# Optimization experiments

Hardware: AMD Instinct MI355X
Metric: run time of the kernel (lower is better)

Reference implementation:

```python
import jax, jax.numpy as jnp
import numpy as np

NUM_HEADS = 16
DIM = 1024


def setup_inputs() -> dict:
    key = jax.random.key(0)
    kx, kw, kb = jax.random.split(key, 3)
    x = jax.random.normal(kx, (4, 2048, DIM), dtype=jnp.float32)
    # torch Linear(dim, 3*dim): weight [3d, d], bias [3d]; store as [d, 3d] for x @ W
    W_qkv = jax.random.normal(kw, (DIM, 3 * DIM), dtype=jnp.float32) * (1.0 / np.sqrt(DIM))
    b_qkv = jax.random.normal(kb, (3 * DIM,), dtype=jnp.float32) * 0.01
    return {"x": x, "W_qkv": W_qkv, "b_qkv": b_qkv}


def reference(x, W_qkv, b_qkv):
    b, t, d = x.shape
    h = NUM_HEADS
    hd = d // h
    qkv = x @ W_qkv + b_qkv  # [b, t, 3d]
    q, k, v = jnp.split(qkv, 3, axis=-1)
    # [b, t, h, hd] -> [b, h, t, hd]
    q = q.reshape(b, t, h, hd).transpose(0, 2, 1, 3)
    k = k.reshape(b, t, h, hd).transpose(0, 2, 1, 3)
    v = v.reshape(b, t, h, hd).transpose(0, 2, 1, 3)
    # NOTE: original scales by sqrt(full dim d), not head_dim
    logits = jnp.einsum("bhqc,bhkc->bhqk", q, k) / jnp.sqrt(jnp.float32(d))
    causal = jnp.tril(jnp.ones((t, t), dtype=bool))  # [t, t]
    logits = jnp.where(causal, logits, -jnp.inf)
    attn = jax.nn.softmax(logits, axis=-1)
    out = jnp.einsum("bhqk,bhkc->bhqc", attn, v)  # [b, h, t, hd]
    return out.transpose(0, 2, 1, 3).reshape(b, t, d)
```

## Files before the change

kernel.cpp:

```cpp
#include <hip/hip_runtime.h>
#include <hip/hip_bf16.h>

#define D_MODEL 1024
#define N3      3072
#define TSEQ    2048
#define M_TOT   8192

typedef __bf16 bf16_8 __attribute__((ext_vector_type(8)));
typedef float  f32x4  __attribute__((ext_vector_type(4)));
typedef short  s16x4  __attribute__((ext_vector_type(4)));

static __device__ __forceinline__ unsigned short f2bf(float f) {
  __hip_bfloat16 h = __float2bfloat16(f);
  unsigned short u;
  __builtin_memcpy(&u, &h, 2);
  return u;
}
static __device__ __forceinline__ unsigned pack2(float lo, float hi) {
  return (unsigned)f2bf(lo) | ((unsigned)f2bf(hi) << 16);
}
static __device__ __forceinline__ void gload16(const void* g, void* l) {
  __builtin_amdgcn_global_load_lds((const __attribute__((address_space(1))) void*)g,
                                   (__attribute__((address_space(3))) void*)l, 16, 0, 0);
}

__global__ void cvt_x_kernel(const float* __restrict__ x, __bf16* __restrict__ xb) {
  size_t i = (size_t)blockIdx.x * 256 + threadIdx.x;
  float4 v = *(const float4*)(x + i * 4);
  ushort4 o;
  o.x = f2bf(v.x); o.y = f2bf(v.y); o.z = f2bf(v.z); o.w = f2bf(v.w);
  *(ushort4*)((unsigned short*)xb + i * 4) = o;
}

__global__ void cvt_w_kernel(const float* __restrict__ W, __bf16* __restrict__ WT) {
  __shared__ unsigned short tl[64][68];
  int t = threadIdx.x;
  int n0 = blockIdx.x * 64, k0 = blockIdx.y * 64;
  int rr = t >> 4, cc = (t & 15) * 4;
#pragma unroll
  for (int i = 0; i < 4; ++i) {
    int r = rr + i * 16;
    float4 v = *(const float4*)(W + (size_t)(k0 + r) * N3 + n0 + cc);
    tl[r][cc] = f2bf(v.x); tl[r][cc + 1] = f2bf(v.y);
    tl[r][cc + 2] = f2bf(v.z); tl[r][cc + 3] = f2bf(v.w);
  }
  __syncthreads();
#pragma unroll
  for (int i = 0; i < 4; ++i) {
    int rc = rr + i * 16;
    ushort4 o;
    o.x = tl[cc + 0][rc]; o.y = tl[cc + 1][rc];
    o.z = tl[cc + 2][rc]; o.w = tl[cc + 3][rc];
    *(ushort4*)((unsigned short*)WT + (size_t)(n0 + rc) * D_MODEL + k0 + cc) = o;
  }
}

__global__ void vtrans_kernel(const __bf16* __restrict__ qkv, __bf16* __restrict__ VT) {
  __shared__ unsigned short tl[64][68];
  int t = threadIdx.x;
  int t0 = blockIdx.x * 64;
  int bh = blockIdx.y;
  int b = bh >> 4, h = bh & 15;
  int rr = t >> 4, cc = (t & 15) * 4;
  const unsigned short* q16 = (const unsigned short*)qkv;
#pragma unroll
  for (int i = 0; i < 4; ++i) {
    int r = rr + i * 16;
    ushort4 v = *(const ushort4*)(q16 + (size_t)(b * TSEQ + t0 + r) * N3 + 2048 + h * 64 + cc);
    tl[r][cc] = v.x; tl[r][cc + 1] = v.y; tl[r][cc + 2] = v.z; tl[r][cc + 3] = v.w;
  }
  __syncthreads();
#pragma unroll
  for (int i = 0; i < 4; ++i) {
    int rc = rr + i * 16;
    ushort4 o;
    o.x = tl[cc + 0][rc]; o.y = tl[cc + 1][rc];
    o.z = tl[cc + 2][rc]; o.w = tl[cc + 3][rc];
    *(ushort4*)((unsigned short*)VT + (size_t)(bh * 64 + rc) * TSEQ + t0 + cc) = o;
  }
}

__global__ __launch_bounds__(256, 2) void gemm_qkv_kernel(
    const __bf16* __restrict__ A, const __bf16* __restrict__ Bt,
    const float* __restrict__ bias, __bf16* __restrict__ C) {
  __shared__ __align__(16) __bf16 Al[4][4096];
  __shared__ __align__(16) __bf16 Bl[4][4096];
  int tid = threadIdx.x;
  int wave = tid >> 6, lane = tid & 63;
  int lr = lane & 15, lg = lane >> 4;
  int m0 = blockIdx.x * 128, n0 = blockIdx.y * 128;
  int wm = (wave >> 1) * 64, wn = (wave & 1) * 64;

  const f32x4 fz = {0.f, 0.f, 0.f, 0.f};
  f32x4 acc[4][4];
#pragma unroll
  for (int i = 0; i < 4; ++i)
#pragma unroll
    for (int j = 0; j < 4; ++j) acc[i][j] = fz;

  auto stage = [&](int buf, int kt) {
#pragma unroll
    for (int call = 0; call < 2; ++call) {
      int cb = call * 256 + wave * 64;
      int c = cb + lane;
      int row = c >> 2;
      int cir = (c & 3) ^ ((row >> 1) & 3);
      gload16(A + (size_t)(m0 + row) * D_MODEL + kt * 32 + cir * 8, &Al[buf][cb * 8]);
      gload16(Bt + (size_t)(n0 + row) * D_MODEL + kt * 32 + cir * 8, &Bl[buf][cb * 8]);
    }
  };

  stage(0, 0); stage(1, 1);
  asm volatile("s_waitcnt vmcnt(4)" ::: "memory");
  __builtin_amdgcn_sched_barrier(0);
  __builtin_amdgcn_s_barrier();

  for (int kt = 0; kt < 32; ++kt) {
    if (kt + 2 < 32) {
      stage((kt + 2) & 3, kt + 2);
      asm volatile("s_waitcnt vmcnt(8)" ::: "memory");
    } else if (kt + 1 < 32) {
      asm volatile("s_waitcnt vmcnt(4)" ::: "memory");
    } else {
      asm volatile("s_waitcnt vmcnt(0)" ::: "memory");
    }
    __builtin_amdgcn_sched_barrier(0);
    __builtin_amdgcn_s_barrier();

    int buf = kt & 3;
    bf16_8 af[4], bv[4];
#pragma unroll
    for (int mb = 0; mb < 4; ++mb) {
      int row = wm + mb * 16 + lr;
      int cir = lg ^ ((row >> 1) & 3);
      af[mb] = *(const bf16_8*)&Al[buf][row * 32 + cir * 8];
    }
#pragma unroll
    for (int nb = 0; nb < 4; ++nb) {
      int row = wn + nb * 16 + lr;
      int cir = lg ^ ((row >> 1) & 3);
      bv[nb] = *(const bf16_8*)&Bl[buf][row * 32 + cir * 8];
    }
    __builtin_amdgcn_s_setprio(1);
#pragma unroll
    for (int mb = 0; mb < 4; ++mb)
#pragma unroll
      for (int nb = 0; nb < 4; ++nb)
        acc[mb][nb] = __builtin_amdgcn_mfma_f32_16x16x32_bf16(af[mb], bv[nb], acc[mb][nb], 0, 0, 0);
    __builtin_amdgcn_s_setprio(0);
  }

  const float SC = 0.04508422f;
  float oscale = (n0 < 1024) ? SC : 1.0f;
  float bvs[4];
#pragma unroll
  for (int nb = 0; nb < 4; ++nb) bvs[nb] = bias[n0 + wn + nb * 16 + lr];
  unsigned short* C16 = (unsigned short*)C;
#pragma unroll
  for (int mb = 0; mb < 4; ++mb)
#pragma unroll
    for (int nb = 0; nb < 4; ++nb)
#pragma unroll
      for (int r = 0; r < 4; ++r) {
        int row = m0 + wm + mb * 16 + lg * 4 + r;
        int col = n0 + wn + nb * 16 + lr;
        C16[(size_t)row * N3 + col] = f2bf((acc[mb][nb][r] + bvs[nb]) * oscale);
      }
}

__global__ __launch_bounds__(256, 4) void attn_kernel(
    const __bf16* __restrict__ qkv, const __bf16* __restrict__ VT,
    float* __restrict__ out) {
  __shared__ __align__(16) char smem[32768];

  int lin = blockIdx.x;
  int y = lin & 63;
  int qt = 31 - (lin >> 6);
  int bh = (y & 7) * 8 + (y >> 3);
  int b = bh >> 4, h = bh & 15;
  int tid = threadIdx.x, wave = tid >> 6, lane = tid & 63;
  int lr = lane & 15, lg = lane >> 4;
  int q0 = qt * 64 + wave * 16;

  const __bf16* Kg = qkv + (size_t)b * TSEQ * N3 + 1024 + h * 64;
  const __bf16* Vg = VT + (size_t)bh * 64 * TSEQ;

  auto stage = [&](int buf, int kv0) {
    __bf16* Kl = (__bf16*)(smem + buf * 16384);
    __bf16* Vl = (__bf16*)(smem + buf * 16384 + 8192);
#pragma unroll
    for (int call = 0; call < 2; ++call) {
      int cb = call * 256 + wave * 64;
      int c = cb + lane;
      int row = c >> 3;
      int cir = (c & 7) ^ (row & 7);
      gload16(Kg + (size_t)(kv0 + row) * N3 + cir * 8, Kl + cb * 8);
      gload16(Vg + (size_t)row * TSEQ + kv0 + cir * 8, Vl + cb * 8);
    }
  };

  bf16_8 qf[2];
#pragma unroll
  for (int kk = 0; kk < 2; ++kk)
    qf[kk] = *(const bf16_8*)&qkv[(size_t)(b * TSEQ + q0 + lr) * N3 + h * 64 + kk * 32 + lg * 8];

  float ps_acc = 0.f;
  const f32x4 fz = {0.f, 0.f, 0.f, 0.f};
  f32x4 oacc[4];
#pragma unroll
  for (int i = 0; i < 4; ++i) oacc[i] = fz;

  int ntiles = qt + 1;
  stage(0, 0);
  asm volatile("s_waitcnt vmcnt(0)" ::: "memory");
  __builtin_amdgcn_sched_barrier(0);
  __builtin_amdgcn_s_barrier();

  for (int tt = 0; tt < ntiles; ++tt) {
    int cur = tt & 1;
    if (tt + 1 < ntiles) stage(cur ^ 1, (tt + 1) * 64);
    __builtin_amdgcn_sched_barrier(0);

    const __bf16* Kb = (const __bf16*)(smem + cur * 16384);
    const __bf16* Vb = (const __bf16*)(smem + cur * 16384 + 8192);
    int kv0 = tt * 64;
    f32x4 st[4];
#pragma unroll
    for (int i = 0; i < 4; ++i) st[i] = fz;
#pragma unroll
    for (int kk = 0; kk < 2; ++kk) {
      bf16_8 kf[4];
#pragma unroll
      for (int mb = 0; mb < 4; ++mb) {
        int row = mb * 16 + lr;
        int cir = (kk * 4 + lg) ^ (row & 7);
        kf[mb] = *(const bf16_8*)&Kb[row * 64 + cir * 8];
      }
      __builtin_amdgcn_s_setprio(1);
#pragma unroll
      for (int mb = 0; mb < 4; ++mb)
        st[mb] = __builtin_amdgcn_mfma_f32_16x16x32_bf16(kf[mb], qf[kk], st[mb], 0, 0, 0);
      __builtin_amdgcn_s_setprio(0);
    }
    unsigned pw[4][2];
    if (kv0 + 63 > q0) {
#pragma unroll
      for (int mb = 0; mb < 4; ++mb) {
        float p[4];
#pragma unroll
        for (int r = 0; r < 4; ++r) {
          int kv = kv0 + mb * 16 + lg * 4 + r;
          float s = (kv > q0 + lr) ? -1e30f : st[mb][r];
          p[r] = __builtin_amdgcn_exp2f(s);
          ps_acc += p[r];
        }
        pw[mb][0] = pack2(p[0], p[1]);
        pw[mb][1] = pack2(p[2], p[3]);
      }
    } else {
#pragma unroll
      for (int mb = 0; mb < 4; ++mb) {
        float p[4];
#pragma unroll
        for (int r = 0; r < 4; ++r) {
          p[r] = __builtin_amdgcn_exp2f(st[mb][r]);
          ps_acc += p[r];
        }
        pw[mb][0] = pack2(p[0], p[1]);
        pw[mb][1] = pack2(p[2], p[3]);
      }
    }
#pragma unroll
    for (int mb = 0; mb < 4; ++mb) {
      s16x4 vf[4];
      int chunk = mb * 2 + (lg >> 1);
#pragma unroll
      for (int mbc = 0; mbc < 4; ++mbc) {
        int row = mbc * 16 + lr;
        int cir = chunk ^ (row & 7);
        vf[mbc] = *(const s16x4*)((const char*)Vb + row * 128 + cir * 16 + (lg & 1) * 8);
      }
      union { unsigned u[2]; s16x4 v; } pf;
      pf.u[0] = pw[mb][0];
      pf.u[1] = pw[mb][1];
      __builtin_amdgcn_s_setprio(1);
#pragma unroll
      for (int mbc = 0; mbc < 4; ++mbc)
        oacc[mbc] = __builtin_amdgcn_mfma_f32_16x16x16bf16_1k(vf[mbc], pf.v, oacc[mbc], 0, 0, 0);
      __builtin_amdgcn_s_setprio(0);
    }

    if (tt + 1 < ntiles) {
      asm volatile("s_waitcnt vmcnt(0)" ::: "memory");
      __builtin_amdgcn_sched_barrier(0);
      __builtin_amdgcn_s_barrier();
    }
  }

  ps_acc += __shfl_xor(ps_acc, 16, 64);
  ps_acc += __shfl_xor(ps_acc, 32, 64);
  float invl = 1.f / ps_acc;
  float* dst = out + (size_t)(b * TSEQ + q0 + lr) * D_MODEL + h * 64 + lg * 4;
#pragma unroll
  for (int mbc = 0; mbc < 4; ++mbc) {
    float4 v;
    v.x = oacc[mbc][0] * invl; v.y = oacc[mbc][1] * invl;
    v.z = oacc[mbc][2] * invl; v.w = oacc[mbc][3] * invl;
    *(float4*)(dst + mbc * 16) = v;
  }
}

extern "C" void kernel_launch(void* const* d_in, const int* in_sizes, int n_in,
                              void* d_out, int out_size, void* d_ws, size_t ws_size,
                              hipStream_t stream) {
  const float* x = (const float*)d_in[0];
  const float* W = (const float*)d_in[1];
  const float* bias = (const float*)d_in[2];
  float* out = (float*)d_out;
  char* ws = (char*)d_ws;
  __bf16* xb  = (__bf16*)(ws);
  __bf16* WT  = (__bf16*)(ws + (size_t)16777216);
  __bf16* qkv = (__bf16*)(ws + (size_t)23068672);
  __bf16* VT  = (__bf16*)(ws + (size_t)73400320);

  hipLaunchKernelGGL(cvt_x_kernel, dim3(8192), dim3(256), 0, stream, x, xb);
  hipLaunchKernelGGL(cvt_w_kernel, dim3(48, 16), dim3(256), 0, stream, W, WT);
  hipLaunchKernelGGL(gemm_qkv_kernel, dim3(64, 24), dim3(256), 0, stream, xb, WT, bias, qkv);
  hipLaunchKernelGGL(vtrans_kernel, dim3(32, 64), dim3(256), 0, stream, qkv, VT);
  hipLaunchKernelGGL(attn_kernel, dim3(2048), dim3(256), 0, stream, qkv, VT, out);
}
```

Baseline: 148.8 us.

## Double attention query tile per block and simplify GEMM pipeline to double buffering

```diff
diff --git a/kernel.cpp b/kernel.cpp
--- a/kernel.cpp
+++ b/kernel.cpp
@@ -83,8 +83,8 @@
 __global__ __launch_bounds__(256, 2) void gemm_qkv_kernel(
     const __bf16* __restrict__ A, const __bf16* __restrict__ Bt,
     const float* __restrict__ bias, __bf16* __restrict__ C) {
-  __shared__ __align__(16) __bf16 Al[4][4096];
-  __shared__ __align__(16) __bf16 Bl[4][4096];
+  __shared__ __align__(16) __bf16 Al[2][4096];
+  __shared__ __align__(16) __bf16 Bl[2][4096];
   int tid = threadIdx.x;
   int wave = tid >> 6, lane = tid & 63;
   int lr = lane & 15, lg = lane >> 4;
@@ -110,24 +110,11 @@
     }
   };
 
-  stage(0, 0); stage(1, 1);
-  asm volatile("s_waitcnt vmcnt(4)" ::: "memory");
-  __builtin_amdgcn_sched_barrier(0);
-  __builtin_amdgcn_s_barrier();
-
+  stage(0, 0);
+  __syncthreads();
   for (int kt = 0; kt < 32; ++kt) {
-    if (kt + 2 < 32) {
-      stage((kt + 2) & 3, kt + 2);
-      asm volatile("s_waitcnt vmcnt(8)" ::: "memory");
-    } else if (kt + 1 < 32) {
-      asm volatile("s_waitcnt vmcnt(4)" ::: "memory");
-    } else {
-      asm volatile("s_waitcnt vmcnt(0)" ::: "memory");
-    }
-    __builtin_amdgcn_sched_barrier(0);
-    __builtin_amdgcn_s_barrier();
-
-    int buf = kt & 3;
+    int buf = kt & 1;
+    if (kt + 1 < 32) stage(buf ^ 1, kt + 1);
     bf16_8 af[4], bv[4];
 #pragma unroll
     for (int mb = 0; mb < 4; ++mb) {
@@ -141,13 +128,12 @@
       int cir = lg ^ ((row >> 1) & 3);
       bv[nb] = *(const bf16_8*)&Bl[buf][row * 32 + cir * 8];
     }
-    __builtin_amdgcn_s_setprio(1);
 #pragma unroll
     for (int mb = 0; mb < 4; ++mb)
 #pragma unroll
       for (int nb = 0; nb < 4; ++nb)
         acc[mb][nb] = __builtin_amdgcn_mfma_f32_16x16x32_bf16(af[mb], bv[nb], acc[mb][nb], 0, 0, 0);
-    __builtin_amdgcn_s_setprio(0);
+    __syncthreads();
   }
 
   const float SC = 0.04508422f;
@@ -175,12 +161,12 @@
 
   int lin = blockIdx.x;
   int y = lin & 63;
-  int qt = 31 - (lin >> 6);
+  int qt = 15 - (lin >> 6);
   int bh = (y & 7) * 8 + (y >> 3);
   int b = bh >> 4, h = bh & 15;
   int tid = threadIdx.x, wave = tid >> 6, lane = tid & 63;
   int lr = lane & 15, lg = lane >> 4;
-  int q0 = qt * 64 + wave * 16;
+  int q0 = qt * 128 + wave * 32;
 
   const __bf16* Kg = qkv + (size_t)b * TSEQ * N3 + 1024 + h * 64;
   const __bf16* Vg = VT + (size_t)bh * 64 * TSEQ;
@@ -199,18 +185,20 @@
     }
   };
 
-  bf16_8 qf[2];
-#pragma unroll
-  for (int kk = 0; kk < 2; ++kk)
-    qf[kk] = *(const bf16_8*)&qkv[(size_t)(b * TSEQ + q0 + lr) * N3 + h * 64 + kk * 32 + lg * 8];
-
-  float ps_acc = 0.f;
+  bf16_8 qf[2][2];
+#pragma unroll
+  for (int nb = 0; nb < 2; ++nb)
+#pragma unroll
+    for (int kk = 0; kk < 2; ++kk)
+      qf[nb][kk] = *(const bf16_8*)&qkv[(size_t)(b * TSEQ + q0 + nb * 16 + lr) * N3 + h * 64 + kk * 32 + lg * 8];
+
+  float ps[2] = {0.f, 0.f};
   const f32x4 fz = {0.f, 0.f, 0.f, 0.f};
-  f32x4 oacc[4];
-#pragma unroll
-  for (int i = 0; i < 4; ++i) oacc[i] = fz;
-
-  int ntiles = qt + 1;
+  f32x4 oacc[4][2];
+#pragma unroll
+  for (int i = 0; i < 4; ++i) { oacc[i][0] = fz; oacc[i][1] = fz; }
+
+  int ntiles = (qt + 1) * 2;
   stage(0, 0);
   asm volatile("s_waitcnt vmcnt(0)" ::: "memory");
   __builtin_amdgcn_sched_barrier(0);
@@ -221,73 +209,85 @@
     if (tt + 1 < ntiles) stage(cur ^ 1, (tt + 1) * 64);
     __builtin_amdgcn_sched_barrier(0);
 
-    const __bf16* Kb = (const __bf16*)(smem + cur * 16384);
-    const __bf16* Vb = (const __bf16*)(smem + cur * 16384 + 8192);
     int kv0 = tt * 64;
-    f32x4 st[4];
-#pragma unroll
-    for (int i = 0; i < 4; ++i) st[i] = fz;
-#pragma unroll
-    for (int kk = 0; kk < 2; ++kk) {
-      bf16_8 kf[4];
+    if (kv0 <= q0 + 31) {
+      const __bf16* Kb = (const __bf16*)(smem + cur * 16384);
+      const __bf16* Vb = (const __bf16*)(smem + cur * 16384 + 8192);
+      f32x4 st[4][2];
+#pragma unroll
+      for (int i = 0; i < 4; ++i) { st[i][0] = fz; st[i][1] = fz; }
+#pragma unroll
+      for (int kk = 0; kk < 2; ++kk) {
+        bf16_8 kf[4];
+#pragma unroll
+        for (int mb = 0; mb < 4; ++mb) {
+          int row = mb * 16 + lr;
+          int cir = (kk * 4 + lg) ^ (row & 7);
+          kf[mb] = *(const bf16_8*)&Kb[row * 64 + cir * 8];
+        }
+        __builtin_amdgcn_s_setprio(1);
+#pragma unroll
+        for (int mb = 0; mb < 4; ++mb)
+#pragma unroll
+          for (int nb = 0; nb < 2; ++nb)
+            st[mb][nb] = __builtin_amdgcn_mfma_f32_16x16x32_bf16(kf[mb], qf[nb][kk], st[mb][nb], 0, 0, 0);
+        __builtin_amdgcn_s_setprio(0);
+      }
+      unsigned pw[4][2][2];
+      if (kv0 + 63 > q0) {
+#pragma unroll
+        for (int mb = 0; mb < 4; ++mb)
+#pragma unroll
+          for (int nb = 0; nb < 2; ++nb) {
+            float p[4];
+            int qq = q0 + nb * 16 + lr;
+#pragma unroll
+            for (int r = 0; r < 4; ++r) {
+              int kv = kv0 + mb * 16 + lg * 4 + r;
+              float s = (kv > qq) ? -1e30f : st[mb][nb][r];
+              p[r] = __builtin_amdgcn_exp2f(s);
+              ps[nb] += p[r];
+            }
+            pw[mb][nb][0] = pack2(p[0], p[1]);
+            pw[mb][nb][1] = pack2(p[2], p[3]);
+          }
+      } else {
+#pragma unroll
+        for (int mb = 0; mb < 4; ++mb)
+#pragma unroll
+          for (int nb = 0; nb < 2; ++nb) {
+            float p[4];
+#pragma unroll
+            for (int r = 0; r < 4; ++r) {
+              p[r] = __builtin_amdgcn_exp2f(st[mb][nb][r]);
+              ps[nb] += p[r];
+            }
+            pw[mb][nb][0] = pack2(p[0], p[1]);
+            pw[mb][nb][1] = pack2(p[2], p[3]);
+          }
+      }
 #pragma unroll
       for (int mb = 0; mb < 4; ++mb) {
-        int row = mb * 16 + lr;
-        int cir = (kk * 4 + lg) ^ (row & 7);
-        kf[mb] = *(const bf16_8*)&Kb[row * 64 + cir * 8];
+        s16x4 vf[4];
+        int chunk = mb * 2 + (lg >> 1);
+#pragma unroll
+        for (int mbc = 0; mbc < 4; ++mbc) {
+          int row = mbc * 16 + lr;
+          int cir = chunk ^ (row & 7);
+          vf[mbc] = *(const s16x4*)((const char*)Vb + row * 128 + cir * 16 + (lg & 1) * 8);
+        }
+        __builtin_amdgcn_s_setprio(1);
+#pragma unroll
+        for (int nb = 0; nb < 2; ++nb) {
+          union { unsigned u[2]; s16x4 v; } pf;
+          pf.u[0] = pw[mb][nb][0];
+          pf.u[1] = pw[mb][nb][1];
+#pragma unroll
+          for (int mbc = 0; mbc < 4; ++mbc)
+            oacc[mbc][nb] = __builtin_amdgcn_mfma_f32_16x16x16bf16_1k(vf[mbc], pf.v, oacc[mbc][nb], 0, 0, 0);
+        }
+        __builtin_amdgcn_s_setprio(0);
       }
-      __builtin_amdgcn_s_setprio(1);
-#pragma unroll
-      for (int mb = 0; mb < 4; ++mb)
-        st[mb] = __builtin_amdgcn_mfma_f32_16x16x32_bf16(kf[mb], qf[kk], st[mb], 0, 0, 0);
-      __builtin_amdgcn_s_setprio(0);
-    }
-    unsigned pw[4][2];
-    if (kv0 + 63 > q0) {
-#pragma unroll
-      for (int mb = 0; mb < 4; ++mb) {
-        float p[4];
-#pragma unroll
-        for (int r = 0; r < 4; ++r) {
-          int kv = kv0 + mb * 16 + lg * 4 + r;
-          float s = (kv > q0 + lr) ? -1e30f : st[mb][r];
-          p[r] = __builtin_amdgcn_exp2f(s);
-          ps_acc += p[r];
-        }
-        pw[mb][0] = pack2(p[0], p[1]);
-        pw[mb][1] = pack2(p[2], p[3]);
-      }
-    } else {
-#pragma unroll
-      for (int mb = 0; mb < 4; ++mb) {
-        float p[4];
-#pragma unroll
-        for (int r = 0; r < 4; ++r) {
-          p[r] = __builtin_amdgcn_exp2f(st[mb][r]);
-          ps_acc += p[r];
-        }
-        pw[mb][0] = pack2(p[0], p[1]);
-        pw[mb][1] = pack2(p[2], p[3]);
-      }
-    }
-#pragma unroll
-    for (int mb = 0; mb < 4; ++mb) {
-      s16x4 vf[4];
-      int chunk = mb * 2 + (lg >> 1);
-#pragma unroll
-      for (int mbc = 0; mbc < 4; ++mbc) {
-        int row = mbc * 16 + lr;
-        int cir = chunk ^ (row & 7);
-        vf[mbc] = *(const s16x4*)((const char*)Vb + row * 128 + cir * 16 + (lg & 1) * 8);
-      }
-      union { unsigned u[2]; s16x4 v; } pf;
-      pf.u[0] = pw[mb][0];
-      pf.u[1] = pw[mb][1];
-      __builtin_amdgcn_s_setprio(1);
-#pragma unroll
-      for (int mbc = 0; mbc < 4; ++mbc)
-        oacc[mbc] = __builtin_amdgcn_mfma_f32_16x16x16bf16_1k(vf[mbc], pf.v, oacc[mbc], 0, 0, 0);
-      __builtin_amdgcn_s_setprio(0);
     }
 
     if (tt + 1 < ntiles) {
@@ -297,16 +297,20 @@
     }
   }
 
-  ps_acc += __shfl_xor(ps_acc, 16, 64);
-  ps_acc += __shfl_xor(ps_acc, 32, 64);
-  float invl = 1.f / ps_acc;
-  float* dst = out + (size_t)(b * TSEQ + q0 + lr) * D_MODEL + h * 64 + lg * 4;
-#pragma unroll
-  for (int mbc = 0; mbc < 4; ++mbc) {
-    float4 v;
-    v.x = oacc[mbc][0] * invl; v.y = oacc[mbc][1] * invl;
-    v.z = oacc[mbc][2] * invl; v.w = oacc[mbc][3] * invl;
-    *(float4*)(dst + mbc * 16) = v;
+#pragma unroll
+  for (int nb = 0; nb < 2; ++nb) {
+    float s = ps[nb];
+    s += __shfl_xor(s, 16, 64);
+    s += __shfl_xor(s, 32, 64);
+    float invl = 1.f / s;
+    float* dst = out + (size_t)(b * TSEQ + q0 + nb * 16 + lr) * D_MODEL + h * 64 + lg * 4;
+#pragma unroll
+    for (int mbc = 0; mbc < 4; ++mbc) {
+      float4 v;
+      v.x = oacc[mbc][nb][0] * invl; v.y = oacc[mbc][nb][1] * invl;
+      v.z = oacc[mbc][nb][2] * invl; v.w = oacc[mbc][nb][3] * invl;
+      *(float4*)(dst + mbc * 16) = v;
+    }
   }
 }
 
@@ -327,5 +331,5 @@
   hipLaunchKernelGGL(cvt_w_kernel, dim3(48, 16), dim3(256), 0, stream, W, WT);
   hipLaunchKernelGGL(gemm_qkv_kernel, dim3(64, 24), dim3(256), 0, stream, xb, WT, bias, qkv);
   hipLaunchKernelGGL(vtrans_kernel, dim3(32, 64), dim3(256), 0, stream, qkv, VT);
-  hipLaunchKernelGGL(attn_kernel, dim3(2048), dim3(256), 0, stream, qkv, VT, out);
-}
+  hipLaunchKernelGGL(attn_kernel, dim3(1024), dim3(256), 0, stream, qkv, VT, out);
+}
```

New measurement: 153.8 us. 1.03x slower.
